# Kernel tuning notes

Measured on AMD Instinct MI355X. Metric: run time of the kernel, lower is better.

The kernel has to match this reference:

```python
import jax, jax.numpy as jnp
import numpy as np

B, K, D = 4, 2048, 512
H, DQ, DV = 8, 64, 64
ATTN_SIZE = 128  # banded local window


def setup_inputs() -> dict:
    key = jax.random.key(0)
    ks = jax.random.split(key, 11)
    s = 1.0 / np.sqrt(D)
    so = 1.0 / np.sqrt(H * DV)
    return {
        "query": jax.random.normal(ks[0], (B, K, D), jnp.float32),
        "key": jax.random.normal(ks[1], (B, K, D), jnp.float32),
        "value": jax.random.normal(ks[2], (B, K, D), jnp.float32),
        "W_q": jax.random.uniform(ks[3], (H * DQ, D), jnp.float32, -s, s),
        "b_q": jax.random.uniform(ks[4], (H * DQ,), jnp.float32, -s, s),
        "W_k": jax.random.uniform(ks[5], (H * DQ, D), jnp.float32, -s, s),
        "b_k": jax.random.uniform(ks[6], (H * DQ,), jnp.float32, -s, s),
        "W_v": jax.random.uniform(ks[7], (H * DV, D), jnp.float32, -s, s),
        "b_v": jax.random.uniform(ks[8], (H * DV,), jnp.float32, -s, s),
        "W_o": jax.random.uniform(ks[9], (D, H * DV), jnp.float32, -so, so),
        "b_o": jax.random.uniform(ks[10], (D,), jnp.float32, -so, so),
    }


def reference(query, key, value, W_q, b_q, W_k, b_k, W_v, b_v, W_o, b_o):
    Klen = query.shape[1]
    # projections; chunk(h, -1) + cat(0) in torch == per-head split of last dim
    q = (query @ W_q.T + b_q).reshape(B, Klen, H, DQ)
    k = (key @ W_k.T + b_k).reshape(B, Klen, H, DQ)
    v = (value @ W_v.T + b_v).reshape(B, Klen, H, DV)
    # NOTE: original scales by sqrt(seq_len K), not sqrt(d_k)
    scores = jnp.einsum('bihq,bjhq->bhij', q, k) / jnp.sqrt(jnp.float32(Klen))
    i = jnp.arange(Klen)[:, None]
    j = jnp.arange(Klen)[None, :]
    # banded local mask (|i-j|<=attention_size) AND causal ('subsequent')
    allowed = (jnp.abs(i - j) <= ATTN_SIZE) & (j <= i)
    scores = jnp.where(allowed, scores, jnp.float32(-jnp.inf))
    probs = jax.nn.softmax(scores, axis=-1)
    attn = jnp.einsum('bhij,bjhv->bihv', probs, v).reshape(B, Klen, H * DV)
    return attn @ W_o.T + b_o
```

## Files before the change

kernel.cpp:

```cpp
#include <hip/hip_runtime.h>
#include <hip/hip_bf16.h>
#include <stdint.h>

#define B_ 4
#define K_ 2048
#define D_ 512
#define H_ 8
#define ATTN_ 128
#define M_ (B_ * K_)

typedef __attribute__((ext_vector_type(4))) float f32x4;
typedef __attribute__((ext_vector_type(8))) short bf16x8;
typedef __attribute__((ext_vector_type(8))) unsigned short u16x8;
typedef __attribute__((ext_vector_type(2))) unsigned int u32x2;

__device__ __forceinline__ unsigned short f2bf(float f) {
    union { float f; unsigned int i; } x; x.f = f;
    unsigned int r = x.i + 0x7fffu + ((x.i >> 16) & 1u);
    return (unsigned short)(r >> 16);
}
__device__ __forceinline__ float bf2f(unsigned short u) {
    union { unsigned int i; float f; } x; x.i = ((unsigned int)u) << 16; return x.f;
}
__device__ __forceinline__ void gload_lds16(const unsigned short* g, unsigned short* l) {
    __builtin_amdgcn_global_load_lds(
        (const __attribute__((address_space(1))) void*)g,
        (__attribute__((address_space(3))) void*)l, 16, 0, 0);
}
__device__ __forceinline__ unsigned lds_addr(const void* p) {
    return (unsigned)(unsigned long long)
        (const __attribute__((address_space(3))) void*)p;
}

struct Cvt { const float* s; unsigned short* d; int n8; };
struct CvtA { Cvt c[4]; };

__global__ __launch_bounds__(256)
void cvt_multi(CvtA a) {
    const Cvt c = a.c[blockIdx.y];
    const float4* s4 = (const float4*)c.s;
    u16x8* d8 = (u16x8*)c.d;
    for (int g = blockIdx.x * 256 + threadIdx.x; g < c.n8; g += gridDim.x * 256) {
        float4 f0 = s4[2 * g], f1 = s4[2 * g + 1];
        u16x8 o;
        o[0] = f2bf(f0.x); o[1] = f2bf(f0.y); o[2] = f2bf(f0.z); o[3] = f2bf(f0.w);
        o[4] = f2bf(f1.x); o[5] = f2bf(f1.y); o[6] = f2bf(f1.z); o[7] = f2bf(f1.w);
        d8[g] = o;
    }
}

struct GArgs {
    const void* A[3];
    const unsigned short* Wt[3];
    const float* bias[3];
    void* C[3];
};

template<bool A_FP32, bool OUT_BF16>
__global__ __launch_bounds__(256, 3)
void gemm_tall(GArgs args)
{
    __shared__ unsigned short As[2][64 * 64];
    __shared__ unsigned short Bs[2][128 * 64];

    const int idf = blockIdx.x;
    const int z   = idf >> 9;
    const int id  = idf & 511;
    const void* Az = args.A[z];
    const unsigned short* Wz = args.Wt[z];
    const float* biz = args.bias[z];
    void* Cz = args.C[z];

    const int x  = id & 7;
    const int i  = id >> 3;
    const int bm = (x * 16 + (i >> 2)) * 64;
    const int bn = (i & 3) * 128;

    const int tid = threadIdx.x;
    const int w   = tid >> 6;
    const int l   = tid & 63;
    const int lr  = l & 15;
    const int lhi = l >> 4;
    const int wm  = (w >> 1) * 32;
    const int wn  = (w & 1) * 64;

    f32x4 acc[2][4];
    #pragma unroll
    for (int a = 0; a < 2; ++a)
        #pragma unroll
        for (int b = 0; b < 4; ++b) acc[a][b] = (f32x4){0.f, 0.f, 0.f, 0.f};

    float4 fa[2][2];

    auto loadA = [&](int t) {
        const int k0 = t * 64;
        #pragma unroll
        for (int it = 0; it < 2; ++it) {
            const int cid = it * 256 + tid;
            const int r = cid >> 3;
            const int c = (cid & 7) ^ (r & 7);
            const float* src = (const float*)Az + (size_t)(bm + r) * D_ + k0 + c * 8;
            fa[it][0] = *(const float4*)src;
            fa[it][1] = *(const float4*)(src + 4);
        }
    };
    auto writeA = [&](int buf) {
        #pragma unroll
        for (int it = 0; it < 2; ++it) {
            const int cid = it * 256 + tid;
            u16x8 o;
            o[0] = f2bf(fa[it][0].x); o[1] = f2bf(fa[it][0].y);
            o[2] = f2bf(fa[it][0].z); o[3] = f2bf(fa[it][0].w);
            o[4] = f2bf(fa[it][1].x); o[5] = f2bf(fa[it][1].y);
            o[6] = f2bf(fa[it][1].z); o[7] = f2bf(fa[it][1].w);
            *(u16x8*)&As[buf][cid * 8] = o;
        }
    };
    auto stageA_bf16 = [&](int buf, int t) {
        const int k0 = t * 64;
        #pragma unroll
        for (int it = 0; it < 2; ++it) {
            const int cg  = it * 4 + w;
            const int cid = cg * 64 + l;
            const int r = cid >> 3;
            const int c = (cid & 7) ^ (r & 7);
            gload_lds16((const unsigned short*)Az + (size_t)(bm + r) * D_ + k0 + c * 8,
                        &As[buf][cg * 512]);
        }
    };
    auto stageB = [&](int buf, int t) {
        const int k0 = t * 64;
        #pragma unroll
        for (int it = 0; it < 4; ++it) {
            const int cg  = it * 4 + w;
            const int cid = cg * 64 + l;
            const int r = cid >> 3;
            const int c = (cid & 7) ^ (r & 7);
            gload_lds16(Wz + (size_t)(bn + r) * D_ + k0 + c * 8,
                        &Bs[buf][cg * 512]);
        }
    };

    if (A_FP32) { loadA(0); writeA(0); }
    else        { stageA_bf16(0, 0); }
    stageB(0, 0);
    __syncthreads();

    int buf = 0;
    for (int t = 0; t < 8; ++t) {
        if (t < 7) {
            if (A_FP32) loadA(t + 1);
            else        stageA_bf16(buf ^ 1, t + 1);
            stageB(buf ^ 1, t + 1);
        }
        #pragma unroll
        for (int kk = 0; kk < 2; ++kk) {
            bf16x8 af[2], bfr[4];
            #pragma unroll
            for (int fm = 0; fm < 2; ++fm) {
                const int row = wm + fm * 16 + lr;
                const int ch  = (kk * 4 + lhi) ^ (lr & 7);
                af[fm] = *(const bf16x8*)&As[buf][row * 64 + ch * 8];
            }
            #pragma unroll
            for (int fn = 0; fn < 4; ++fn) {
                const int row = wn + fn * 16 + lr;
                const int ch  = (kk * 4 + lhi) ^ (lr & 7);
                bfr[fn] = *(const bf16x8*)&Bs[buf][row * 64 + ch * 8];
            }
            #pragma unroll
            for (int fm = 0; fm < 2; ++fm)
                #pragma unroll
                for (int fn = 0; fn < 4; ++fn)
                    acc[fm][fn] = __builtin_amdgcn_mfma_f32_16x16x32_bf16(
                        af[fm], bfr[fn], acc[fm][fn], 0, 0, 0);
        }
        if (A_FP32 && t < 7) writeA(buf ^ 1);
        __syncthreads();
        buf ^= 1;
    }

    float bv[4];
    #pragma unroll
    for (int fn = 0; fn < 4; ++fn) bv[fn] = biz[bn + wn + fn * 16 + lr];

    #pragma unroll
    for (int fm = 0; fm < 2; ++fm)
        #pragma unroll
        for (int fn = 0; fn < 4; ++fn)
            #pragma unroll
            for (int rr = 0; rr < 4; ++rr) {
                const int row = bm + wm + fm * 16 + lhi * 4 + rr;
                const int col = bn + wn + fn * 16 + lr;
                const float val = acc[fm][fn][rr] + bv[fn];
                if (OUT_BF16)
                    ((unsigned short*)Cz)[(size_t)row * 512 + col] = f2bf(val);
                else
                    ((float*)Cz)[(size_t)row * 512 + col] = val;
            }
}

__global__ __launch_bounds__(256)
void attn_mfma(const unsigned short* __restrict__ qb,
               const unsigned short* __restrict__ kb,
               const unsigned short* __restrict__ vb,
               unsigned short* __restrict__ ob)
{
    __shared__ unsigned short Ksh[192 * 64];
    __shared__ unsigned short Vsh[4 * 192 * 16];
    __shared__ unsigned short Psh[4 * 16 * 200];

    const int flat = blockIdx.x + 32 * (blockIdx.y + 8 * blockIdx.z);
    const int lg   = (flat & 7) * 128 + (flat >> 3);
    const int tile = lg & 31;
    const int h    = (lg >> 5) & 7;
    const int b    = lg >> 8;

    const int i0 = tile * 64;
    const int j0 = i0 - 128;
    const int tid = threadIdx.x;
    const int w   = tid >> 6;
    const int l   = tid & 63;
    const int lr  = l & 15;
    const int lhi = l >> 4;
    const float scale = 0.0220970869120796f;

    const size_t hbase = ((size_t)b * K_) * 512 + (size_t)h * 64;
    const unsigned short* kh = kb + hbase;
    const unsigned short* vh = vb + hbase;
    const unsigned short* qh = qb + hbase;
    unsigned short* oh = ob + hbase;

    #pragma unroll
    for (int it = 0; it < 6; ++it) {
        const int cg  = it * 4 + w;
        const int cid = cg * 64 + l;
        const int r = cid >> 3, c = cid & 7;
        const int cs = c ^ (r & 7);
        int j = j0 + r; if (j < 0) j = 0;
        gload_lds16(kh + (size_t)j * 512 + cs * 8, &Ksh[cg * 64 * 8]);
    }
    #pragma unroll
    for (int it = 0; it < 6; ++it) {
        const int cg  = it * 4 + w;
        const int cid = cg * 64 + l;
        const int blk = cid / 384;
        const int rem = cid - blk * 384;
        const int prow = rem >> 1, hf = rem & 1;
        const int a = prow >> 2, bb = prow & 3;
        const int k = (a < 24) ? (8 * a + bb) : (8 * (a - 24) + 4 + bb);
        int j = j0 + k; if (j < 0) j = 0;
        gload_lds16(vh + (size_t)j * 512 + blk * 16 + hf * 8, &Vsh[cg * 64 * 8]);
    }

    bf16x8 qa[2];
    {
        const unsigned short* qrow = qh + (size_t)(i0 + 16 * w + lr) * 512;
        qa[0] = *(const bf16x8*)(qrow + lhi * 8);
        qa[1] = *(const bf16x8*)(qrow + 32 + lhi * 8);
    }
    __syncthreads();

    const int jcbase = w & ~1;
    f32x4 sacc[10];
    #pragma unroll
    for (int jc = 0; jc < 10; ++jc) sacc[jc] = (f32x4){0.f, 0.f, 0.f, 0.f};

    __builtin_amdgcn_s_setprio(1);
    #pragma unroll
    for (int kk = 0; kk < 2; ++kk) {
        const int ch = (kk * 4 + lhi) ^ (lr & 7);
        #pragma unroll
        for (int jc = 0; jc < 10; ++jc) {
            const int row = (jcbase + jc) * 16 + lr;
            bf16x8 kf = *(const bf16x8*)&Ksh[row * 64 + ch * 8];
            sacc[jc] = __builtin_amdgcn_mfma_f32_16x16x32_bf16(
                qa[kk], kf, sacc[jc], 0, 0, 0);
        }
    }
    __builtin_amdgcn_s_setprio(0);

    unsigned short* myP = &Psh[w * 3200];
    const int lo0 = 128 - i0;
    float lsum[4] = {0.f, 0.f, 0.f, 0.f};
    #pragma unroll
    for (int jc = 0; jc < 10; ++jc) {
        const int jcol = (jcbase + jc) * 16 + lr;
        #pragma unroll
        for (int rr = 0; rr < 4; ++rr) {
            const int iloc = 16 * w + 4 * lhi + rr;
            const bool ok = (jcol >= iloc) && (jcol <= iloc + ATTN_) && (jcol >= lo0);
            const float p = ok ? __expf(fminf(sacc[jc][rr] * scale, 80.f)) : 0.f;
            lsum[rr] += p;
            myP[(4 * lhi + rr) * 200 + jcol] = f2bf(p);
        }
    }
    #pragma unroll
    for (int rr = 0; rr < 4; ++rr) {
        float s = lsum[rr];
        s += __shfl_xor(s, 1, 16);
        s += __shfl_xor(s, 2, 16);
        s += __shfl_xor(s, 4, 16);
        s += __shfl_xor(s, 8, 16);
        lsum[rr] = s;
    }

    const int kcbase = w >> 1;
    f32x4 oacc[4];
    #pragma unroll
    for (int fn = 0; fn < 4; ++fn) oacc[fn] = (f32x4){0.f, 0.f, 0.f, 0.f};
    const unsigned vbase = lds_addr(&Vsh[0]) + (unsigned)(l * 8);

    for (int kc5 = 0; kc5 < 5; ++kc5) {
        const int kc = kcbase + kc5;
        bf16x8 pa = *(const bf16x8*)&myP[lr * 200 + kc * 32 + lhi * 8];
        u32x2 vlo[4], vhi[4];
        #pragma unroll
        for (int fn = 0; fn < 4; ++fn) {
            const unsigned addr = vbase + (unsigned)((fn * 3072 + kc * 256) * 2);
            asm volatile("ds_read_b64_tr_b16 %0, %1" : "=v"(vlo[fn]) : "v"(addr));
            asm volatile("ds_read_b64_tr_b16 %0, %1 offset:3072"
                         : "=v"(vhi[fn]) : "v"(addr));
        }
        asm volatile("s_waitcnt lgkmcnt(0)" ::: "memory");
        __builtin_amdgcn_sched_barrier(0);
        __builtin_amdgcn_s_setprio(1);
        #pragma unroll
        for (int fn = 0; fn < 4; ++fn) {
            union { u32x2 h[2]; bf16x8 v; } u;
            u.h[0] = vlo[fn]; u.h[1] = vhi[fn];
            oacc[fn] = __builtin_amdgcn_mfma_f32_16x16x32_bf16(
                pa, u.v, oacc[fn], 0, 0, 0);
        }
        __builtin_amdgcn_s_setprio(0);
    }

    float inv[4];
    #pragma unroll
    for (int rr = 0; rr < 4; ++rr) inv[rr] = 1.f / lsum[rr];
    #pragma unroll
    for (int fn = 0; fn < 4; ++fn)
        #pragma unroll
        for (int rr = 0; rr < 4; ++rr) {
            const int row = i0 + 16 * w + 4 * lhi + rr;
            oh[(size_t)row * 512 + fn * 16 + lr] = f2bf(oacc[fn][rr] * inv[rr]);
        }
}

extern "C" void kernel_launch(void* const* d_in, const int* in_sizes, int n_in,
                              void* d_out, int out_size, void* d_ws, size_t ws_size,
                              hipStream_t stream)
{
    const float* query = (const float*)d_in[0];
    const float* key   = (const float*)d_in[1];
    const float* value = (const float*)d_in[2];
    const float* W_q   = (const float*)d_in[3];
    const float* b_q   = (const float*)d_in[4];
    const float* W_k   = (const float*)d_in[5];
    const float* b_k   = (const float*)d_in[6];
    const float* W_v   = (const float*)d_in[7];
    const float* b_v   = (const float*)d_in[8];
    const float* W_o   = (const float*)d_in[9];
    const float* b_o   = (const float*)d_in[10];
    float* out = (float*)d_out;

    const size_t NX = (size_t)M_ * 512;
    const size_t NW = 512 * 512;
    unsigned short* wqb = (unsigned short*)d_ws;
    unsigned short* wkb = wqb + NW;
    unsigned short* wvb = wkb + NW;
    unsigned short* wob = wvb + NW;
    unsigned short* qp  = wob + NW;
    unsigned short* kp  = qp + NX;
    unsigned short* vp  = kp + NX;
    unsigned short* ap  = vp + NX;

    const int NW8 = (int)(NW / 8);

    CvtA a;
    a.c[0] = { W_q, wqb, NW8 };
    a.c[1] = { W_k, wkb, NW8 };
    a.c[2] = { W_v, wvb, NW8 };
    a.c[3] = { W_o, wob, NW8 };
    cvt_multi<<<dim3(32, 4), 256, 0, stream>>>(a);

    GArgs qa;
    qa.A[0] = query; qa.A[1] = key; qa.A[2] = value;
    qa.Wt[0] = wqb;  qa.Wt[1] = wkb; qa.Wt[2] = wvb;
    qa.bias[0] = b_q; qa.bias[1] = b_k; qa.bias[2] = b_v;
    qa.C[0] = qp; qa.C[1] = kp; qa.C[2] = vp;
    gemm_tall<true, true><<<1536, 256, 0, stream>>>(qa);

    attn_mfma<<<dim3(32, 8, 4), 256, 0, stream>>>(qp, kp, vp, ap);

    GArgs oa;
    oa.A[0] = ap; oa.A[1] = nullptr; oa.A[2] = nullptr;
    oa.Wt[0] = wob; oa.Wt[1] = nullptr; oa.Wt[2] = nullptr;
    oa.bias[0] = b_o; oa.bias[1] = nullptr; oa.bias[2] = nullptr;
    oa.C[0] = out; oa.C[1] = nullptr; oa.C[2] = nullptr;
    gemm_tall<false, false><<<512, 256, 0, stream>>>(oa);
}
```

Baseline: 61.05 us.

## Replace 64x128 GEMM tiles with 256x256 tiles and interleaved load/MFMA schedule

Rewrites the projection GEMMs to use 512-thread blocks, each computing a 256x256 output tile, so fewer blocks (192 for QKV, 64 for output) each get more operand reuse. Global-to-LDS staging for the next K-step is interleaved between MFMA phases using explicit barriers and s_setprio, and blocks are remapped with an XCD-aware swizzle. The risk is low occupancy: only 192 or 64 blocks on a 256-CU GPU leave CUs idle, and the large accumulator array raises register pressure.

New measurement: 70.05 us. +14.8%, slower.

```diff
diff --git a/kernel.cpp b/kernel.cpp
--- a/kernel.cpp
+++ b/kernel.cpp
@@ -57,127 +57,135 @@
 };
 
 template<bool A_FP32, bool OUT_BF16>
-__global__ __launch_bounds__(256, 3)
-void gemm_tall(GArgs args)
+__global__ __launch_bounds__(512)
+void gemm256(GArgs args)
 {
-    __shared__ unsigned short As[2][64 * 64];
-    __shared__ unsigned short Bs[2][128 * 64];
-
-    const int idf = blockIdx.x;
-    const int z   = idf >> 9;
-    const int id  = idf & 511;
+    __shared__ unsigned short As[2][256 * 64];
+    __shared__ unsigned short Bs[2][256 * 64];
+
+    const int id  = blockIdx.x;
+    const int cpx = gridDim.x >> 3;
+    const int swz = (id & 7) * cpx + (id >> 3);
+    const int mt  = swz >> 1;
+    const int nt  = swz & 1;
+    const int z   = mt >> 5;
+    const int bm  = (mt & 31) * 256;
+    const int bn  = nt * 256;
+
     const void* Az = args.A[z];
     const unsigned short* Wz = args.Wt[z];
     const float* biz = args.bias[z];
     void* Cz = args.C[z];
-
-    const int x  = id & 7;
-    const int i  = id >> 3;
-    const int bm = (x * 16 + (i >> 2)) * 64;
-    const int bn = (i & 3) * 128;
 
     const int tid = threadIdx.x;
     const int w   = tid >> 6;
     const int l   = tid & 63;
     const int lr  = l & 15;
     const int lhi = l >> 4;
-    const int wm  = (w >> 1) * 32;
-    const int wn  = (w & 1) * 64;
-
-    f32x4 acc[2][4];
-    #pragma unroll
-    for (int a = 0; a < 2; ++a)
-        #pragma unroll
-        for (int b = 0; b < 4; ++b) acc[a][b] = (f32x4){0.f, 0.f, 0.f, 0.f};
-
-    float4 fa[2][2];
-
-    auto loadA = [&](int t) {
-        const int k0 = t * 64;
-        #pragma unroll
-        for (int it = 0; it < 2; ++it) {
-            const int cid = it * 256 + tid;
+    const int wm  = (w >> 2) * 128;
+    const int wn  = (w & 3) * 64;
+
+    f32x4 acc[8][4];
+    #pragma unroll
+    for (int m = 0; m < 8; ++m)
+        #pragma unroll
+        for (int n = 0; n < 4; ++n) acc[m][n] = (f32x4){0.f, 0.f, 0.f, 0.f};
+
+    float4 fa[4][2];
+
+    auto loadA_f32 = [&](int t) {
+        #pragma unroll
+        for (int q = 0; q < 4; ++q) {
+            const int cid = q * 512 + tid;
             const int r = cid >> 3;
             const int c = (cid & 7) ^ (r & 7);
-            const float* src = (const float*)Az + (size_t)(bm + r) * D_ + k0 + c * 8;
-            fa[it][0] = *(const float4*)src;
-            fa[it][1] = *(const float4*)(src + 4);
+            const float* src = (const float*)Az + (size_t)(bm + r) * D_ + t * 64 + c * 8;
+            fa[q][0] = *(const float4*)src;
+            fa[q][1] = *(const float4*)(src + 4);
         }
     };
-    auto writeA = [&](int buf) {
-        #pragma unroll
-        for (int it = 0; it < 2; ++it) {
-            const int cid = it * 256 + tid;
+    auto writeA_f32 = [&](int buf) {
+        #pragma unroll
+        for (int q = 0; q < 4; ++q) {
+            const int cid = q * 512 + tid;
             u16x8 o;
-            o[0] = f2bf(fa[it][0].x); o[1] = f2bf(fa[it][0].y);
-            o[2] = f2bf(fa[it][0].z); o[3] = f2bf(fa[it][0].w);
-            o[4] = f2bf(fa[it][1].x); o[5] = f2bf(fa[it][1].y);
-            o[6] = f2bf(fa[it][1].z); o[7] = f2bf(fa[it][1].w);
+            o[0] = f2bf(fa[q][0].x); o[1] = f2bf(fa[q][0].y);
+            o[2] = f2bf(fa[q][0].z); o[3] = f2bf(fa[q][0].w);
+            o[4] = f2bf(fa[q][1].x); o[5] = f2bf(fa[q][1].y);
+            o[6] = f2bf(fa[q][1].z); o[7] = f2bf(fa[q][1].w);
             *(u16x8*)&As[buf][cid * 8] = o;
         }
     };
-    auto stageA_bf16 = [&](int buf, int t) {
-        const int k0 = t * 64;
-        #pragma unroll
-        for (int it = 0; it < 2; ++it) {
-            const int cg  = it * 4 + w;
-            const int cid = cg * 64 + l;
+    auto stageA_b16 = [&](int buf, int t) {
+        #pragma unroll
+        for (int q = 0; q < 4; ++q) {
+            const int cid = q * 512 + tid;
             const int r = cid >> 3;
             const int c = (cid & 7) ^ (r & 7);
-            gload_lds16((const unsigned short*)Az + (size_t)(bm + r) * D_ + k0 + c * 8,
-                        &As[buf][cg * 512]);
+            gload_lds16((const unsigned short*)Az + (size_t)(bm + r) * D_ + t * 64 + c * 8,
+                        &As[buf][(q * 512 + w * 64) * 8]);
         }
     };
     auto stageB = [&](int buf, int t) {
-        const int k0 = t * 64;
-        #pragma unroll
-        for (int it = 0; it < 4; ++it) {
-            const int cg  = it * 4 + w;
-            const int cid = cg * 64 + l;
+        #pragma unroll
+        for (int q = 0; q < 4; ++q) {
+            const int cid = q * 512 + tid;
             const int r = cid >> 3;
             const int c = (cid & 7) ^ (r & 7);
-            gload_lds16(Wz + (size_t)(bn + r) * D_ + k0 + c * 8,
-                        &Bs[buf][cg * 512]);
+            gload_lds16(Wz + (size_t)(bn + r) * D_ + t * 64 + c * 8,
+                        &Bs[buf][(q * 512 + w * 64) * 8]);
         }
     };
 
-    if (A_FP32) { loadA(0); writeA(0); }
-    else        { stageA_bf16(0, 0); }
+    if (A_FP32) { loadA_f32(0); writeA_f32(0); }
+    else        { stageA_b16(0, 0); }
     stageB(0, 0);
     __syncthreads();
 
-    int buf = 0;
     for (int t = 0; t < 8; ++t) {
-        if (t < 7) {
-            if (A_FP32) loadA(t + 1);
-            else        stageA_bf16(buf ^ 1, t + 1);
-            stageB(buf ^ 1, t + 1);
-        }
+        const int buf = t & 1;
         #pragma unroll
         for (int kk = 0; kk < 2; ++kk) {
-            bf16x8 af[2], bfr[4];
+            bf16x8 af[8];
             #pragma unroll
-            for (int fm = 0; fm < 2; ++fm) {
-                const int row = wm + fm * 16 + lr;
-                const int ch  = (kk * 4 + lhi) ^ (lr & 7);
-                af[fm] = *(const bf16x8*)&As[buf][row * 64 + ch * 8];
+            for (int m = 0; m < 8; ++m) {
+                const int row = wm + m * 16 + lr;
+                const int sl  = (kk * 4 + lhi) ^ (row & 7);
+                af[m] = *(const bf16x8*)&As[buf][row * 64 + sl * 8];
             }
             #pragma unroll
-            for (int fn = 0; fn < 4; ++fn) {
-                const int row = wn + fn * 16 + lr;
-                const int ch  = (kk * 4 + lhi) ^ (lr & 7);
-                bfr[fn] = *(const bf16x8*)&Bs[buf][row * 64 + ch * 8];
+            for (int nh = 0; nh < 2; ++nh) {
+                bf16x8 bfr[2];
+                #pragma unroll
+                for (int n2 = 0; n2 < 2; ++n2) {
+                    const int row = wn + (nh * 2 + n2) * 16 + lr;
+                    const int sl  = (kk * 4 + lhi) ^ (row & 7);
+                    bfr[n2] = *(const bf16x8*)&Bs[buf][row * 64 + sl * 8];
+                }
+                const int p = kk * 2 + nh;
+                if (t < 7) {
+                    if (p == 0) {
+                        if (A_FP32) loadA_f32(t + 1);
+                        else        stageA_b16(buf ^ 1, t + 1);
+                    } else if (p == 1) {
+                        stageB(buf ^ 1, t + 1);
+                    } else if (p == 3 && A_FP32) {
+                        writeA_f32(buf ^ 1);
+                    }
+                }
+                __builtin_amdgcn_s_barrier();
+                __builtin_amdgcn_s_setprio(1);
+                #pragma unroll
+                for (int m = 0; m < 8; ++m)
+                    #pragma unroll
+                    for (int n2 = 0; n2 < 2; ++n2)
+                        acc[m][nh * 2 + n2] = __builtin_amdgcn_mfma_f32_16x16x32_bf16(
+                            af[m], bfr[n2], acc[m][nh * 2 + n2], 0, 0, 0);
+                __builtin_amdgcn_s_setprio(0);
+                if (p < 3) __builtin_amdgcn_s_barrier();
             }
-            #pragma unroll
-            for (int fm = 0; fm < 2; ++fm)
-                #pragma unroll
-                for (int fn = 0; fn < 4; ++fn)
-                    acc[fm][fn] = __builtin_amdgcn_mfma_f32_16x16x32_bf16(
-                        af[fm], bfr[fn], acc[fm][fn], 0, 0, 0);
-        }
-        if (A_FP32 && t < 7) writeA(buf ^ 1);
+        }
         __syncthreads();
-        buf ^= 1;
     }
 
     float bv[4];
@@ -185,14 +193,14 @@
     for (int fn = 0; fn < 4; ++fn) bv[fn] = biz[bn + wn + fn * 16 + lr];
 
     #pragma unroll
-    for (int fm = 0; fm < 2; ++fm)
+    for (int m = 0; m < 8; ++m)
         #pragma unroll
         for (int fn = 0; fn < 4; ++fn)
             #pragma unroll
             for (int rr = 0; rr < 4; ++rr) {
-                const int row = bm + wm + fm * 16 + lhi * 4 + rr;
+                const int row = bm + wm + m * 16 + lhi * 4 + rr;
                 const int col = bn + wn + fn * 16 + lr;
-                const float val = acc[fm][fn][rr] + bv[fn];
+                const float val = acc[m][fn][rr] + bv[fn];
                 if (OUT_BF16)
                     ((unsigned short*)Cz)[(size_t)row * 512 + col] = f2bf(val);
                 else
@@ -389,14 +397,14 @@
     qa.Wt[0] = wqb;  qa.Wt[1] = wkb; qa.Wt[2] = wvb;
     qa.bias[0] = b_q; qa.bias[1] = b_k; qa.bias[2] = b_v;
     qa.C[0] = qp; qa.C[1] = kp; qa.C[2] = vp;
-    gemm_tall<true, true><<<1536, 256, 0, stream>>>(qa);
+    gemm256<true, true><<<192, 512, 0, stream>>>(qa);
 
     attn_mfma<<<dim3(32, 8, 4), 256, 0, stream>>>(qp, kp, vp, ap);
 
     GArgs oa;
-    oa.A[0] = ap; oa.A[1] = nullptr; oa.A[2] = nullptr;
-    oa.Wt[0] = wob; oa.Wt[1] = nullptr; oa.Wt[2] = nullptr;
-    oa.bias[0] = b_o; oa.bias[1] = nullptr; oa.bias[2] = nullptr;
-    oa.C[0] = out; oa.C[1] = nullptr; oa.C[2] = nullptr;
-    gemm_tall<false, false><<<512, 256, 0, stream>>>(oa);
-}
+    oa.A[0] = ap; oa.A[1] = ap; oa.A[2] = ap;
+    oa.Wt[0] = wob; oa.Wt[1] = wob; oa.Wt[2] = wob;
+    oa.bias[0] = b_o; oa.bias[1] = b_o; oa.bias[2] = b_o;
+    oa.C[0] = out; oa.C[1] = out; oa.C[2] = out;
+    gemm256<false, false><<<64, 512, 0, stream>>>(oa);
+}
```
